# Optimization experiments

Hardware: AMD Instinct MI355X
Metric: run time of the kernel (lower is better)

## Reference

```python
import jax, jax.numpy as jnp
import numpy as np


def setup_inputs() -> dict:
    key = jax.random.key(0)
    k1, k2, k3, k4 = jax.random.split(key, 4)
    B, T, D, L = 32, 30, 512, 196
    x = jax.random.normal(k1, (B, T, D), dtype=jnp.float32)
    wordemb = jax.random.normal(k2, (B, T, D), dtype=jnp.float32)
    imgsfeats = jax.random.normal(k3, (B, L, D), dtype=jnp.float32)
    v_w = jax.random.normal(k4, (D,), dtype=jnp.float32) * (1.0 / np.sqrt(D))
    v_b = jnp.zeros((1,), dtype=jnp.float32)
    return {"x": x, "wordemb": wordemb, "imgsfeats": imgsfeats, "v_w": v_w, "v_b": v_b}


def reference(x, wordemb, imgsfeats, v_w, v_b):
    # x, wordemb: (B, T=30, D=512); imgsfeats: (B, L, D)
    # y = imgsfeats.transpose(2,1) broadcast over T: (B, 1, D, L)
    y = jnp.transpose(imgsfeats, (0, 2, 1))[:, None, :, :]          # (B,1,D,L)
    att = jnp.tanh(x[:, :, :, None] + y + wordemb[:, :, :, None])   # (B,T,D,L)
    # score: linear D->1 applied along D
    e = jnp.einsum('btdl,d->btl', att, v_w) + v_b[0]                 # (B,T,L)
    alpha = jax.nn.softmax(e, axis=-1)                               # (B,T,L)
    # context = sum_l y * alpha -> (B,T,D)
    context = jnp.einsum('bld,btl->btd', imgsfeats, alpha)
    return context
```

## Files before the change

kernel.cpp:

```cpp
#include <hip/hip_runtime.h>

namespace {
constexpr int kB = 32, kT = 30, kD = 512, kL = 196;
constexpr float kK = 2.8853900817779268f;
constexpr size_t kGsz = (size_t)kB * kT * kL;

#define PAIR(ex, ey, fx, fy, vx, vy, acc)                                   \
  {                                                                         \
    const float u_ = fmaf(ex, fx, 1.f);                                     \
    const float v_ = fmaf(ey, fy, 1.f);                                     \
    acc = fmaf(fmaf(v_, vx, u_ * vy), __builtin_amdgcn_rcpf(u_ * v_), acc); \
  }

__global__ __launch_bounds__(512) void k_score(const float* __restrict__ x,
                                               const float* __restrict__ w,
                                               const float* __restrict__ img,
                                               const float* __restrict__ vw,
                                               float* __restrict__ g8) {
  __shared__ __align__(16) float4 Fl4[16 * 64];
  __shared__ __align__(16) float4 El4[32 * 16];
  __shared__ __align__(16) float4 vwl4[16];
  __shared__ __align__(16) float sc[4 * 8 * 64];
  int n = blockIdx.x;
  const int bg = n & 7;
  int m = n >> 3;
  const int bi = m & 3; m >>= 2;
  const int lc = m % 3;
  const int dqg = m / 3;
  const int b = bg * 4 + bi;
  const int l0 = lc * 64, d0 = dqg * 64;
  const int tid = threadIdx.x;
#pragma unroll
  for (int k = 0; k < 2; ++k) {
    const int i = tid + k * 512;
    const int l = i >> 4, c = i & 15;
    const float4 v =
        *(const float4*)(img + ((size_t)(b * kL + l0 + l)) * kD + d0 + 4 * c);
    float4 o;
    o.x = __builtin_amdgcn_exp2f(kK * v.x);
    o.y = __builtin_amdgcn_exp2f(kK * v.y);
    o.z = __builtin_amdgcn_exp2f(kK * v.z);
    o.w = __builtin_amdgcn_exp2f(kK * v.w);
    Fl4[c * 64 + (l ^ (c & 7))] = o;
  }
  {
    const int row = tid >> 4, c4 = tid & 15;
    const int tc = (row < kT) ? row : kT - 1;
    const size_t gi = ((size_t)(b * kT + tc)) * kD + d0 + 4 * c4;
    const float4 xv = *(const float4*)(x + gi);
    const float4 wv4 = *(const float4*)(w + gi);
    float4 e;
    e.x = __builtin_amdgcn_exp2f(kK * (xv.x + wv4.x));
    e.y = __builtin_amdgcn_exp2f(kK * (xv.y + wv4.y));
    e.z = __builtin_amdgcn_exp2f(kK * (xv.z + wv4.z));
    e.w = __builtin_amdgcn_exp2f(kK * (xv.w + wv4.w));
    El4[row * 16 + c4] = e;
  }
  if (tid < 16) vwl4[tid] = *(const float4*)(vw + d0 + 4 * tid);
  __syncthreads();
  const int lane = tid & 63, wva = tid >> 6;
  const int tg = wva & 3, dh = wva >> 2;
  const int r0 = tg * 8;
  const float4* Ew = &El4[r0 * 16];
  float acc[8];
#pragma unroll
  for (int tt = 0; tt < 8; ++tt) acc[tt] = 0.f;
#pragma unroll
  for (int s = 0; s < 8; ++s) {
    const int c4 = dh * 8 + s;
    const float4 f = Fl4[c4 * 64 + (lane ^ s)];
    const float4 vv = vwl4[c4];
#pragma unroll
    for (int tt = 0; tt < 8; ++tt) {
      const float4 E = Ew[tt * 16 + c4];
      PAIR(E.x, E.y, f.x, f.y, vv.x, vv.y, acc[tt]);
      PAIR(E.z, E.w, f.z, f.w, vv.z, vv.w, acc[tt]);
    }
  }
  if (dh == 1) {
#pragma unroll
    for (int tt = 0; tt < 8; ++tt) sc[(tg * 8 + tt) * 64 + lane] = acc[tt];
  }
  __syncthreads();
  if (dh == 0) {
    float* gp =
        g8 + (size_t)dqg * kGsz + ((size_t)(b * kT + r0)) * kL + l0 + lane;
#pragma unroll
    for (int tt = 0; tt < 8; ++tt) {
      if (r0 + tt < kT) {
        gp[(size_t)tt * kL] = acc[tt] + sc[(tg * 8 + tt) * 64 + lane];
      }
    }
  }
}

__global__ __launch_bounds__(512) void k_alpha(const float* __restrict__ g8,
                                               const float* __restrict__ x,
                                               const float* __restrict__ w,
                                               const float* __restrict__ img,
                                               const float* __restrict__ vw,
                                               float* __restrict__ alpha) {
  const int qd = blockIdx.x, b = blockIdx.y;
  const int lane = threadIdx.x & 63, wv = threadIdx.x >> 6;
  const int t = qd * 8 + wv;
  if (t >= kT) return;
  const int l4 = lane & 3, dc = lane >> 2;
  const float* ir = img + ((size_t)(b * kL + 192 + l4)) * kD + dc * 32;
  const float* xr = x + ((size_t)(b * kT + t)) * kD + dc * 32;
  const float* wr = w + ((size_t)(b * kT + t)) * kD + dc * 32;
  const float* vr = vw + dc * 32;
  float tg = 0.f;
#pragma unroll
  for (int k = 0; k < 8; ++k) {
    const float4 iv = *(const float4*)(ir + 4 * k);
    const float4 xv = *(const float4*)(xr + 4 * k);
    const float4 wv4 = *(const float4*)(wr + 4 * k);
    const float4 vv = *(const float4*)(vr + 4 * k);
    const float fx = __builtin_amdgcn_exp2f(kK * iv.x);
    const float fy = __builtin_amdgcn_exp2f(kK * iv.y);
    const float fz = __builtin_amdgcn_exp2f(kK * iv.z);
    const float fw = __builtin_amdgcn_exp2f(kK * iv.w);
    const float ex = __builtin_amdgcn_exp2f(kK * (xv.x + wv4.x));
    const float ey = __builtin_amdgcn_exp2f(kK * (xv.y + wv4.y));
    const float ez = __builtin_amdgcn_exp2f(kK * (xv.z + wv4.z));
    const float ew = __builtin_amdgcn_exp2f(kK * (xv.w + wv4.w));
    PAIR(ex, ey, fx, fy, vv.x, vv.y, tg);
    PAIR(ez, ew, fz, fw, vv.z, vv.w, tg);
  }
#pragma unroll
  for (int mm = 4; mm < 64; mm <<= 1) tg += __shfl_xor(tg, mm, 64);
  const size_t base = ((size_t)(b * kT + t)) * kL;
  float q0 = 0.f, q1 = 0.f, q2 = 0.f;
#pragma unroll
  for (int p = 0; p < 8; ++p) {
    const float* gp = g8 + (size_t)p * kGsz + base;
    q0 += gp[lane];
    q1 += gp[lane + 64];
    q2 += gp[lane + 128];
  }
  q0 *= kK; q1 *= kK; q2 *= kK;
  float q3 = (lane < 4) ? tg * kK : __builtin_inff();
  float m = fminf(fminf(q0, q1), fminf(q2, q3));
#pragma unroll
  for (int mm = 1; mm < 64; mm <<= 1) m = fminf(m, __shfl_xor(m, mm, 64));
  const float e0 = __builtin_amdgcn_exp2f(m - q0);
  const float e1 = __builtin_amdgcn_exp2f(m - q1);
  const float e2 = __builtin_amdgcn_exp2f(m - q2);
  const float e3 = (lane < 4) ? __builtin_amdgcn_exp2f(m - q3) : 0.f;
  float s = e0 + e1 + e2 + e3;
#pragma unroll
  for (int mm = 1; mm < 64; mm <<= 1) s += __shfl_xor(s, mm, 64);
  const float rs = __builtin_amdgcn_rcpf(s);
  float* ab = alpha + base;
  ab[lane] = e0 * rs;
  ab[lane + 64] = e1 * rs;
  ab[lane + 128] = e2 * rs;
  if (lane < 4) ab[lane + 192] = e3 * rs;
}

__global__ __launch_bounds__(256) void k_ctx(const float* __restrict__ img,
                                             const float* __restrict__ alpha,
                                             float* __restrict__ out) {
  __shared__ __align__(16) float red[4][5][256];
  int n = blockIdx.x;
  const int bg = n & 7;
  int m = n >> 3;
  const int bi = m & 3; m >>= 2;
  const int tg = m % 6;
  const int dh = m / 6;
  const int b = bg * 4 + bi;
  const int t0 = tg * 5, d0 = dh * 256;
  const int tid = threadIdx.x;
  const int lane = tid & 63;
  const int lru = __builtin_amdgcn_readfirstlane(tid >> 6);
  const float* ap = alpha + ((size_t)(b * kT + t0)) * kL + lru * 49;
  const float* ip = img + ((size_t)(b * kL + lru * 49)) * kD + d0 + 4 * lane;
  float4 acc[5];
#pragma unroll
  for (int j = 0; j < 5; ++j) acc[j] = {0.f, 0.f, 0.f, 0.f};
  auto loadI = [&](float4* dst, int bb) {
#pragma unroll
    for (int j = 0; j < 8; ++j)
      dst[j] = *(const float4*)(ip + (size_t)(bb * 8 + j) * kD);
  };
  auto compI = [&](const float4* f, int bb) {
#pragma unroll
    for (int j = 0; j < 8; ++j) {
      const int i = bb * 8 + j;
      const float a0 = ap[i];
      const float a1 = ap[kL + i];
      const float a2 = ap[2 * kL + i];
      const float a3 = ap[3 * kL + i];
      const float a4 = ap[4 * kL + i];
      acc[0].x = fmaf(f[j].x, a0, acc[0].x); acc[0].y = fmaf(f[j].y, a0, acc[0].y);
      acc[0].z = fmaf(f[j].z, a0, acc[0].z); acc[0].w = fmaf(f[j].w, a0, acc[0].w);
      acc[1].x = fmaf(f[j].x, a1, acc[1].x); acc[1].y = fmaf(f[j].y, a1, acc[1].y);
      acc[1].z = fmaf(f[j].z, a1, acc[1].z); acc[1].w = fmaf(f[j].w, a1, acc[1].w);
      acc[2].x = fmaf(f[j].x, a2, acc[2].x); acc[2].y = fmaf(f[j].y, a2, acc[2].y);
      acc[2].z = fmaf(f[j].z, a2, acc[2].z); acc[2].w = fmaf(f[j].w, a2, acc[2].w);
      acc[3].x = fmaf(f[j].x, a3, acc[3].x); acc[3].y = fmaf(f[j].y, a3, acc[3].y);
      acc[3].z = fmaf(f[j].z, a3, acc[3].z); acc[3].w = fmaf(f[j].w, a3, acc[3].w);
      acc[4].x = fmaf(f[j].x, a4, acc[4].x); acc[4].y = fmaf(f[j].y, a4, acc[4].y);
      acc[4].z = fmaf(f[j].z, a4, acc[4].z); acc[4].w = fmaf(f[j].w, a4, acc[4].w);
    }
  };
  float4 fA[8], fB[8];
  loadI(fA, 0);
  loadI(fB, 1); compI(fA, 0);
  loadI(fA, 2); compI(fB, 1);
  loadI(fB, 3); compI(fA, 2);
  loadI(fA, 4); compI(fB, 3);
  loadI(fB, 5); compI(fA, 4);
  compI(fB, 5);
  {
    const float4 v = *(const float4*)(ip + (size_t)48 * kD);
    const int i = 48;
    const float a0 = ap[i], a1 = ap[kL + i], a2 = ap[2 * kL + i],
                a3 = ap[3 * kL + i], a4 = ap[4 * kL + i];
    acc[0].x = fmaf(v.x, a0, acc[0].x); acc[0].y = fmaf(v.y, a0, acc[0].y);
    acc[0].z = fmaf(v.z, a0, acc[0].z); acc[0].w = fmaf(v.w, a0, acc[0].w);
    acc[1].x = fmaf(v.x, a1, acc[1].x); acc[1].y = fmaf(v.y, a1, acc[1].y);
    acc[1].z = fmaf(v.z, a1, acc[1].z); acc[1].w = fmaf(v.w, a1, acc[1].w);
    acc[2].x = fmaf(v.x, a2, acc[2].x); acc[2].y = fmaf(v.y, a2, acc[2].y);
    acc[2].z = fmaf(v.z, a2, acc[2].z); acc[2].w = fmaf(v.w, a2, acc[2].w);
    acc[3].x = fmaf(v.x, a3, acc[3].x); acc[3].y = fmaf(v.y, a3, acc[3].y);
    acc[3].z = fmaf(v.z, a3, acc[3].z); acc[3].w = fmaf(v.w, a3, acc[3].w);
    acc[4].x = fmaf(v.x, a4, acc[4].x); acc[4].y = fmaf(v.y, a4, acc[4].y);
    acc[4].z = fmaf(v.z, a4, acc[4].z); acc[4].w = fmaf(v.w, a4, acc[4].w);
  }
#pragma unroll
  for (int j = 0; j < 5; ++j) *(float4*)&red[lru][j][4 * lane] = acc[j];
  __syncthreads();
#pragma unroll
  for (int j = 0; j < 5; ++j) {
    const float s =
        red[0][j][tid] + red[1][j][tid] + red[2][j][tid] + red[3][j][tid];
    out[((size_t)(b * kT + t0 + j)) * kD + d0 + tid] = s;
  }
}
}

extern "C" void kernel_launch(void* const* d_in, const int* in_sizes, int n_in,
                              void* d_out, int out_size, void* d_ws, size_t ws_size,
                              hipStream_t stream) {
  const float* x = (const float*)d_in[0];
  const float* wordemb = (const float*)d_in[1];
  const float* img = (const float*)d_in[2];
  const float* vw = (const float*)d_in[3];
  float* out = (float*)d_out;
  float* g8 = (float*)d_ws;
  float* alpha = g8 + 8 * kGsz;
  hipLaunchKernelGGL(k_score, dim3(768), dim3(512), 0, stream, x, wordemb, img,
                     vw, g8);
  hipLaunchKernelGGL(k_alpha, dim3(4, kB), dim3(512), 0, stream, g8, x, wordemb,
                     img, vw, alpha);
  hipLaunchKernelGGL(k_ctx, dim3(384), dim3(256), 0, stream, img, alpha, out);
}
```

Baseline: 31.14 us.

## Fuse softmax alpha computation into context kernel via shared memory

Removes the separate alpha kernel. Each context block now computes softmax weights for its 5 time steps directly into shared memory, then uses them for the weighted sum over image features. This saves a kernel launch and the global round trip for alpha. In exchange, the softmax work is repeated across the two d-halves, and wave 0 handles two rows serially before the barrier. The image prefetch chunk also shrinks from 8 to 4 rows to lower register pressure.

```diff
diff --git a/kernel.cpp b/kernel.cpp
--- a/kernel.cpp
+++ b/kernel.cpp
@@ -94,73 +94,13 @@
   }
 }
 
-__global__ __launch_bounds__(512) void k_alpha(const float* __restrict__ g8,
-                                               const float* __restrict__ x,
-                                               const float* __restrict__ w,
-                                               const float* __restrict__ img,
-                                               const float* __restrict__ vw,
-                                               float* __restrict__ alpha) {
-  const int qd = blockIdx.x, b = blockIdx.y;
-  const int lane = threadIdx.x & 63, wv = threadIdx.x >> 6;
-  const int t = qd * 8 + wv;
-  if (t >= kT) return;
-  const int l4 = lane & 3, dc = lane >> 2;
-  const float* ir = img + ((size_t)(b * kL + 192 + l4)) * kD + dc * 32;
-  const float* xr = x + ((size_t)(b * kT + t)) * kD + dc * 32;
-  const float* wr = w + ((size_t)(b * kT + t)) * kD + dc * 32;
-  const float* vr = vw + dc * 32;
-  float tg = 0.f;
-#pragma unroll
-  for (int k = 0; k < 8; ++k) {
-    const float4 iv = *(const float4*)(ir + 4 * k);
-    const float4 xv = *(const float4*)(xr + 4 * k);
-    const float4 wv4 = *(const float4*)(wr + 4 * k);
-    const float4 vv = *(const float4*)(vr + 4 * k);
-    const float fx = __builtin_amdgcn_exp2f(kK * iv.x);
-    const float fy = __builtin_amdgcn_exp2f(kK * iv.y);
-    const float fz = __builtin_amdgcn_exp2f(kK * iv.z);
-    const float fw = __builtin_amdgcn_exp2f(kK * iv.w);
-    const float ex = __builtin_amdgcn_exp2f(kK * (xv.x + wv4.x));
-    const float ey = __builtin_amdgcn_exp2f(kK * (xv.y + wv4.y));
-    const float ez = __builtin_amdgcn_exp2f(kK * (xv.z + wv4.z));
-    const float ew = __builtin_amdgcn_exp2f(kK * (xv.w + wv4.w));
-    PAIR(ex, ey, fx, fy, vv.x, vv.y, tg);
-    PAIR(ez, ew, fz, fw, vv.z, vv.w, tg);
-  }
-#pragma unroll
-  for (int mm = 4; mm < 64; mm <<= 1) tg += __shfl_xor(tg, mm, 64);
-  const size_t base = ((size_t)(b * kT + t)) * kL;
-  float q0 = 0.f, q1 = 0.f, q2 = 0.f;
-#pragma unroll
-  for (int p = 0; p < 8; ++p) {
-    const float* gp = g8 + (size_t)p * kGsz + base;
-    q0 += gp[lane];
-    q1 += gp[lane + 64];
-    q2 += gp[lane + 128];
-  }
-  q0 *= kK; q1 *= kK; q2 *= kK;
-  float q3 = (lane < 4) ? tg * kK : __builtin_inff();
-  float m = fminf(fminf(q0, q1), fminf(q2, q3));
-#pragma unroll
-  for (int mm = 1; mm < 64; mm <<= 1) m = fminf(m, __shfl_xor(m, mm, 64));
-  const float e0 = __builtin_amdgcn_exp2f(m - q0);
-  const float e1 = __builtin_amdgcn_exp2f(m - q1);
-  const float e2 = __builtin_amdgcn_exp2f(m - q2);
-  const float e3 = (lane < 4) ? __builtin_amdgcn_exp2f(m - q3) : 0.f;
-  float s = e0 + e1 + e2 + e3;
-#pragma unroll
-  for (int mm = 1; mm < 64; mm <<= 1) s += __shfl_xor(s, mm, 64);
-  const float rs = __builtin_amdgcn_rcpf(s);
-  float* ab = alpha + base;
-  ab[lane] = e0 * rs;
-  ab[lane + 64] = e1 * rs;
-  ab[lane + 128] = e2 * rs;
-  if (lane < 4) ab[lane + 192] = e3 * rs;
-}
-
-__global__ __launch_bounds__(256) void k_ctx(const float* __restrict__ img,
-                                             const float* __restrict__ alpha,
-                                             float* __restrict__ out) {
+__global__ __launch_bounds__(256) void k_ctxa(const float* __restrict__ g8,
+                                              const float* __restrict__ x,
+                                              const float* __restrict__ w,
+                                              const float* __restrict__ img,
+                                              const float* __restrict__ vw,
+                                              float* __restrict__ out) {
+  __shared__ float AL2[5][200];
   __shared__ __align__(16) float red[4][5][256];
   int n = blockIdx.x;
   const int bg = n & 7;
@@ -172,26 +112,83 @@
   const int t0 = tg * 5, d0 = dh * 256;
   const int tid = threadIdx.x;
   const int lane = tid & 63;
-  const int lru = __builtin_amdgcn_readfirstlane(tid >> 6);
-  const float* ap = alpha + ((size_t)(b * kT + t0)) * kL + lru * 49;
+  const int wv = tid >> 6;
+#pragma unroll 1
+  for (int r = wv; r < 5; r += 4) {
+    const int t = t0 + r;
+    const int l4 = lane & 3, dc = lane >> 2;
+    const float* ir = img + ((size_t)(b * kL + 192 + l4)) * kD + dc * 32;
+    const float* xr = x + ((size_t)(b * kT + t)) * kD + dc * 32;
+    const float* wr = w + ((size_t)(b * kT + t)) * kD + dc * 32;
+    const float* vr = vw + dc * 32;
+    float tgv = 0.f;
+#pragma unroll
+    for (int k = 0; k < 8; ++k) {
+      const float4 iv = *(const float4*)(ir + 4 * k);
+      const float4 xv = *(const float4*)(xr + 4 * k);
+      const float4 wv4 = *(const float4*)(wr + 4 * k);
+      const float4 vv = *(const float4*)(vr + 4 * k);
+      const float fx = __builtin_amdgcn_exp2f(kK * iv.x);
+      const float fy = __builtin_amdgcn_exp2f(kK * iv.y);
+      const float fz = __builtin_amdgcn_exp2f(kK * iv.z);
+      const float fw = __builtin_amdgcn_exp2f(kK * iv.w);
+      const float ex = __builtin_amdgcn_exp2f(kK * (xv.x + wv4.x));
+      const float ey = __builtin_amdgcn_exp2f(kK * (xv.y + wv4.y));
+      const float ez = __builtin_amdgcn_exp2f(kK * (xv.z + wv4.z));
+      const float ew = __builtin_amdgcn_exp2f(kK * (xv.w + wv4.w));
+      PAIR(ex, ey, fx, fy, vv.x, vv.y, tgv);
+      PAIR(ez, ew, fz, fw, vv.z, vv.w, tgv);
+    }
+#pragma unroll
+    for (int mm = 4; mm < 64; mm <<= 1) tgv += __shfl_xor(tgv, mm, 64);
+    const size_t base = ((size_t)(b * kT + t)) * kL;
+    float q0 = 0.f, q1 = 0.f, q2 = 0.f;
+#pragma unroll
+    for (int p = 0; p < 8; ++p) {
+      const float* gp = g8 + (size_t)p * kGsz + base;
+      q0 += gp[lane];
+      q1 += gp[lane + 64];
+      q2 += gp[lane + 128];
+    }
+    q0 *= kK; q1 *= kK; q2 *= kK;
+    float q3 = (lane < 4) ? tgv * kK : __builtin_inff();
+    float mn = fminf(fminf(q0, q1), fminf(q2, q3));
+#pragma unroll
+    for (int mm = 1; mm < 64; mm <<= 1) mn = fminf(mn, __shfl_xor(mn, mm, 64));
+    const float e0 = __builtin_amdgcn_exp2f(mn - q0);
+    const float e1 = __builtin_amdgcn_exp2f(mn - q1);
+    const float e2 = __builtin_amdgcn_exp2f(mn - q2);
+    const float e3 = (lane < 4) ? __builtin_amdgcn_exp2f(mn - q3) : 0.f;
+    float s = e0 + e1 + e2 + e3;
+#pragma unroll
+    for (int mm = 1; mm < 64; mm <<= 1) s += __shfl_xor(s, mm, 64);
+    const float rs = __builtin_amdgcn_rcpf(s);
+    AL2[r][lane] = e0 * rs;
+    AL2[r][lane + 64] = e1 * rs;
+    AL2[r][lane + 128] = e2 * rs;
+    if (lane < 4) AL2[r][lane + 192] = e3 * rs;
+  }
+  __syncthreads();
+  const int lru = __builtin_amdgcn_readfirstlane(wv);
   const float* ip = img + ((size_t)(b * kL + lru * 49)) * kD + d0 + 4 * lane;
+  const int lb = lru * 49;
   float4 acc[5];
 #pragma unroll
   for (int j = 0; j < 5; ++j) acc[j] = {0.f, 0.f, 0.f, 0.f};
   auto loadI = [&](float4* dst, int bb) {
 #pragma unroll
-    for (int j = 0; j < 8; ++j)
-      dst[j] = *(const float4*)(ip + (size_t)(bb * 8 + j) * kD);
+    for (int j = 0; j < 4; ++j)
+      dst[j] = *(const float4*)(ip + (size_t)(bb * 4 + j) * kD);
   };
   auto compI = [&](const float4* f, int bb) {
 #pragma unroll
-    for (int j = 0; j < 8; ++j) {
-      const int i = bb * 8 + j;
-      const float a0 = ap[i];
-      const float a1 = ap[kL + i];
-      const float a2 = ap[2 * kL + i];
-      const float a3 = ap[3 * kL + i];
-      const float a4 = ap[4 * kL + i];
+    for (int j = 0; j < 4; ++j) {
+      const int l = lb + bb * 4 + j;
+      const float a0 = AL2[0][l];
+      const float a1 = AL2[1][l];
+      const float a2 = AL2[2][l];
+      const float a3 = AL2[3][l];
+      const float a4 = AL2[4][l];
       acc[0].x = fmaf(f[j].x, a0, acc[0].x); acc[0].y = fmaf(f[j].y, a0, acc[0].y);
       acc[0].z = fmaf(f[j].z, a0, acc[0].z); acc[0].w = fmaf(f[j].w, a0, acc[0].w);
       acc[1].x = fmaf(f[j].x, a1, acc[1].x); acc[1].y = fmaf(f[j].y, a1, acc[1].y);
@@ -204,19 +201,22 @@
       acc[4].z = fmaf(f[j].z, a4, acc[4].z); acc[4].w = fmaf(f[j].w, a4, acc[4].w);
     }
   };
-  float4 fA[8], fB[8];
+  float4 fA[4], fB[4];
   loadI(fA, 0);
-  loadI(fB, 1); compI(fA, 0);
-  loadI(fA, 2); compI(fB, 1);
-  loadI(fB, 3); compI(fA, 2);
-  loadI(fA, 4); compI(fB, 3);
-  loadI(fB, 5); compI(fA, 4);
-  compI(fB, 5);
+#pragma unroll
+  for (int bb = 0; bb < 12; ++bb) {
+    if (bb + 1 < 12) {
+      if ((bb + 1) & 1) loadI(fB, bb + 1);
+      else loadI(fA, bb + 1);
+    }
+    if (bb & 1) compI(fB, bb);
+    else compI(fA, bb);
+  }
   {
     const float4 v = *(const float4*)(ip + (size_t)48 * kD);
-    const int i = 48;
-    const float a0 = ap[i], a1 = ap[kL + i], a2 = ap[2 * kL + i],
-                a3 = ap[3 * kL + i], a4 = ap[4 * kL + i];
+    const int l = lb + 48;
+    const float a0 = AL2[0][l], a1 = AL2[1][l], a2 = AL2[2][l],
+                a3 = AL2[3][l], a4 = AL2[4][l];
     acc[0].x = fmaf(v.x, a0, acc[0].x); acc[0].y = fmaf(v.y, a0, acc[0].y);
     acc[0].z = fmaf(v.z, a0, acc[0].z); acc[0].w = fmaf(v.w, a0, acc[0].w);
     acc[1].x = fmaf(v.x, a1, acc[1].x); acc[1].y = fmaf(v.y, a1, acc[1].y);
@@ -229,7 +229,7 @@
     acc[4].z = fmaf(v.z, a4, acc[4].z); acc[4].w = fmaf(v.w, a4, acc[4].w);
   }
 #pragma unroll
-  for (int j = 0; j < 5; ++j) *(float4*)&red[lru][j][4 * lane] = acc[j];
+  for (int j = 0; j < 5; ++j) *(float4*)&red[wv][j][4 * lane] = acc[j];
   __syncthreads();
 #pragma unroll
   for (int j = 0; j < 5; ++j) {
@@ -249,10 +249,8 @@
   const float* vw = (const float*)d_in[3];
   float* out = (float*)d_out;
   float* g8 = (float*)d_ws;
-  float* alpha = g8 + 8 * kGsz;
   hipLaunchKernelGGL(k_score, dim3(768), dim3(512), 0, stream, x, wordemb, img,
                      vw, g8);
-  hipLaunchKernelGGL(k_alpha, dim3(4, kB), dim3(512), 0, stream, g8, x, wordemb,
-                     img, vw, alpha);
-  hipLaunchKernelGGL(k_ctx, dim3(384), dim3(256), 0, stream, img, alpha, out);
-}
+  hipLaunchKernelGGL(k_ctxa, dim3(384), dim3(256), 0, stream, g8, x, wordemb,
+                     img, vw, out);
+}
```

Result: faster. 28.71 us (median of 2 runs) (-7.8%).
